# Performance work log

Measured on AMD Instinct MI355X. Metric: run time of the kernel, lower is better.

## Reference

```python
import jax, jax.numpy as jnp
import numpy as np

EMBED = 768
NUM_HEADS = 12
HEAD_DIM = EMBED // NUM_HEADS
SCALE = HEAD_DIM ** -0.5


def setup_inputs() -> dict:
    key = jax.random.key(0)
    ks = jax.random.split(key, 12)
    B, H, W = 1, 48, 48
    L = 2 * H - 1
    s = EMBED ** -0.5
    return {
        "hidden_states": jax.random.normal(ks[0], (B, H, W, EMBED), jnp.float32),
        "wq": jax.random.normal(ks[1], (EMBED, EMBED), jnp.float32) * s,
        "bq": jax.random.normal(ks[2], (EMBED,), jnp.float32) * 0.02,
        "wk": jax.random.normal(ks[3], (EMBED, EMBED), jnp.float32) * s,
        "bk": jax.random.normal(ks[4], (EMBED,), jnp.float32) * 0.02,
        "wv": jax.random.normal(ks[5], (EMBED, EMBED), jnp.float32) * s,
        "bv": jax.random.normal(ks[6], (EMBED,), jnp.float32) * 0.02,
        "wproj": jax.random.normal(ks[7], (EMBED, EMBED), jnp.float32) * s,
        "bproj": jax.random.normal(ks[8], (EMBED,), jnp.float32) * 0.02,
        "rel_pos_h": jax.random.normal(ks[9], (L, HEAD_DIM), jnp.float32) * 0.02,
        "rel_pos_w": jax.random.normal(ks[10], (L, HEAD_DIM), jnp.float32) * 0.02,
    }


def _get_rel_pos(q_size, k_size, rel_pos):
    # q_size == k_size here; table already has 2*size-1 entries (no interp)
    q = jnp.arange(q_size)[:, None]
    k = jnp.arange(k_size)[None, :]
    idx = q - k + (k_size - 1)  # (q_size, k_size)
    return rel_pos[idx]  # (q_size, k_size, head_dim)


def reference(hidden_states, wq, bq, wk, bk, wv, bv, wproj, bproj, rel_pos_h, rel_pos_w):
    B, H, W, C = hidden_states.shape
    nH, hd = NUM_HEADS, HEAD_DIM
    HW = H * W

    def proj_heads(w, b):
        # 1x1 conv == linear: (B,H,W,C) -> (B*nH, HW, hd)
        y = jnp.einsum("bhwc,oc->bhwo", hidden_states, w) + b
        return y.reshape(B, HW, nH, hd).transpose(0, 2, 1, 3).reshape(B * nH, HW, hd)

    q = proj_heads(wq, bq)
    k = proj_heads(wk, bk)
    v = proj_heads(wv, bv)

    scores = jnp.einsum("bqd,bkd->bqk", q * SCALE, k)  # (B*nH, HW, HW)

    Rh = _get_rel_pos(H, H, rel_pos_h)  # (H,H,hd)
    Rw = _get_rel_pos(W, W, rel_pos_w)  # (W,W,hd)
    qr = q.reshape(B * nH, H, W, hd)
    rel_h = jnp.einsum("bhwc,hkc->bhwk", qr, Rh)  # (B*nH,H,W,H)
    rel_w = jnp.einsum("bhwc,wkc->bhwk", qr, Rw)  # (B*nH,H,W,W)
    bias = rel_h[:, :, :, :, None] + rel_w[:, :, :, None, :]
    scores = scores + bias.reshape(B * nH, HW, HW)

    attn = jax.nn.softmax(scores.astype(jnp.float32), axis=-1).astype(q.dtype)
    out = jnp.einsum("bqk,bkd->bqd", attn, v)  # (B*nH, HW, hd)
    out = out.reshape(B, nH, H, W, hd).transpose(0, 2, 3, 1, 4).reshape(B, H, W, C)
    out = jnp.einsum("bhwc,oc->bhwo", out, wproj) + bproj
    return out, attn
```

## Files before the change

### kernel.cpp

```cpp
#include <hip/hip_runtime.h>
#include <math.h>

#define EMBED 768
#define NH 12
#define HD 64
#define HWTOK 2304
#define SCALE 0.125f

typedef unsigned short ushort_t;
typedef __attribute__((ext_vector_type(8))) short short8v;
typedef __attribute__((ext_vector_type(4))) short short4v;
typedef __attribute__((ext_vector_type(4))) float f32x4;

__device__ __forceinline__ unsigned short f2bf(float f) {
  unsigned u = __float_as_uint(f);
  u += 0x7fffu + ((u >> 16) & 1u);
  return (unsigned short)(u >> 16);
}
__device__ __forceinline__ float bf2f(unsigned short h) {
  return __uint_as_float(((unsigned)h) << 16);
}

__device__ __forceinline__ void split2(float a, float b, unsigned& hi, unsigned& lo) {
  unsigned ua = __float_as_uint(a), ub = __float_as_uint(b);
  unsigned ra = ua + 0x7fffu + ((ua >> 16) & 1u);
  unsigned rb = ub + 0x7fffu + ((ub >> 16) & 1u);
  float ha = __uint_as_float(ra & 0xffff0000u);
  float hb = __uint_as_float(rb & 0xffff0000u);
  hi = (ra >> 16) | (rb & 0xffff0000u);
  unsigned la = __float_as_uint(a - ha);
  unsigned lb = __float_as_uint(b - hb);
  lo = (la >> 16) | (lb & 0xffff0000u);
}

__global__ __launch_bounds__(256)
void split_kernel(const float* __restrict__ src, ushort_t* __restrict__ dh,
                  ushort_t* __restrict__ dl, int n4) {
  int i = blockIdx.x * 256 + threadIdx.x;
  int stride = gridDim.x * 256;
  for (; i < n4; i += stride) {
    float4 v = ((const float4*)src)[i];
    unsigned h0, l0, h1, l1;
    split2(v.x, v.y, h0, l0);
    split2(v.z, v.w, h1, l1);
    *(uint2*)&dh[(size_t)i * 4] = make_uint2(h0, h1);
    *(uint2*)&dl[(size_t)i * 4] = make_uint2(l0, l1);
  }
}

__device__ __forceinline__ void stage16(const float* __restrict__ src, char* dh, char* dl,
                                        int b0, int rs) {
  const float4* s4 = (const float4*)src;
  float4 f0 = s4[0], f1 = s4[1], f2 = s4[2], f3 = s4[3];
  uint4 H0, L0, H1, L1;
  split2(f0.x, f0.y, H0.x, L0.x); split2(f0.z, f0.w, H0.y, L0.y);
  split2(f1.x, f1.y, H0.z, L0.z); split2(f1.z, f1.w, H0.w, L0.w);
  split2(f2.x, f2.y, H1.x, L1.x); split2(f2.z, f2.w, H1.y, L1.y);
  split2(f3.x, f3.y, H1.z, L1.z); split2(f3.z, f3.w, H1.w, L1.w);
  *(uint4*)(dh + (b0 ^ rs))        = H0;
  *(uint4*)(dh + ((b0 + 16) ^ rs)) = H1;
  *(uint4*)(dl + (b0 ^ rs))        = L0;
  *(uint4*)(dl + ((b0 + 16) ^ rs)) = L1;
}

template<int IN_F32, int OUT_MODE>
__global__ __launch_bounds__(256)
void gemm_bf3(const ushort_t* __restrict__ Ah, const ushort_t* __restrict__ Al,
              const float* __restrict__ Af, const float* __restrict__ W,
              const float* __restrict__ bias, float* __restrict__ Y,
              ushort_t* __restrict__ Yh, ushort_t* __restrict__ Yl,
              int M, int N, int K) {
  __shared__ __align__(16) char smem[32768];

  const int tid  = threadIdx.x;
  const int w    = tid >> 6;
  const int lane = tid & 63;
  const int u    = lane >> 4;
  const int cc   = lane & 15;
  const int mw   = w >> 1, nw = w & 1;
  const int m0   = blockIdx.y * 64;
  const int n0   = blockIdx.x * 64;
  const int sr   = tid >> 2;
  const int sq   = tid & 3;
  const int srs  = (sr & 7) << 4;

  char* sAh_w = smem;
  char* sAl_w = smem + 8192;
  char* sWh_w = smem + 16384;
  char* sWl_w = smem + 24576;
  const int swzc = (cc & 7) << 4;

  f32x4 acc[2][2];
#pragma unroll
  for (int i = 0; i < 2; ++i)
#pragma unroll
    for (int j = 0; j < 2; ++j) acc[i][j] = (f32x4){0.f, 0.f, 0.f, 0.f};

  for (int k0 = 0; k0 < K; k0 += 64) {
    __syncthreads();
    if (IN_F32) {
      stage16(&Af[(size_t)(m0 + sr) * K + k0 + sq * 16],
              sAh_w + sr * 128, sAl_w + sr * 128, sq * 32, srs);
    } else {
      const ushort_t* ap = &Ah[(size_t)(m0 + sr) * K + k0 + sq * 16];
      const ushort_t* lp = &Al[(size_t)(m0 + sr) * K + k0 + sq * 16];
      uint4 h0 = *(const uint4*)ap;
      uint4 h1 = *(const uint4*)(ap + 8);
      uint4 l0 = *(const uint4*)lp;
      uint4 l1 = *(const uint4*)(lp + 8);
      *(uint4*)(sAh_w + sr * 128 + ((sq * 32) ^ srs))      = h0;
      *(uint4*)(sAh_w + sr * 128 + ((sq * 32 + 16) ^ srs)) = h1;
      *(uint4*)(sAl_w + sr * 128 + ((sq * 32) ^ srs))      = l0;
      *(uint4*)(sAl_w + sr * 128 + ((sq * 32 + 16) ^ srs)) = l1;
    }
    stage16(&W[(size_t)(n0 + sr) * K + k0 + sq * 16],
            sWh_w + sr * 128, sWl_w + sr * 128, sq * 32, srs);
    __syncthreads();

#pragma unroll
    for (int k2 = 0; k2 < 2; ++k2) {
      const int ko = k2 * 64;
      short8v a_h[2], a_l[2], b_h[2], b_l[2];
#pragma unroll
      for (int i = 0; i < 2; ++i) {
        int off = (32 * mw + 16 * i + cc) * 128 + ((u * 16 + ko) ^ swzc);
        a_h[i] = *(const short8v*)(sAh_w + off);
        a_l[i] = *(const short8v*)(sAl_w + off);
      }
#pragma unroll
      for (int j = 0; j < 2; ++j) {
        int off = (32 * nw + 16 * j + cc) * 128 + ((u * 16 + ko) ^ swzc);
        b_h[j] = *(const short8v*)(sWh_w + off);
        b_l[j] = *(const short8v*)(sWl_w + off);
      }
#pragma unroll
      for (int i = 0; i < 2; ++i)
#pragma unroll
        for (int j = 0; j < 2; ++j) {
          acc[i][j] = __builtin_amdgcn_mfma_f32_16x16x32_bf16(a_h[i], b_h[j], acc[i][j], 0, 0, 0);
          acc[i][j] = __builtin_amdgcn_mfma_f32_16x16x32_bf16(a_h[i], b_l[j], acc[i][j], 0, 0, 0);
          acc[i][j] = __builtin_amdgcn_mfma_f32_16x16x32_bf16(a_l[i], b_h[j], acc[i][j], 0, 0, 0);
        }
    }
  }

  __syncthreads();
  float* Cs = (float*)smem;
#pragma unroll
  for (int i = 0; i < 2; ++i)
#pragma unroll
    for (int j = 0; j < 2; ++j)
#pragma unroll
      for (int r = 0; r < 4; ++r)
        Cs[(32 * mw + 16 * i + 4 * u + r) * 68 + 32 * nw + 16 * j + cc] = acc[i][j][r];
  __syncthreads();

  {
    int rr = tid >> 2, cg = (tid & 3) * 16;
    float v[16];
#pragma unroll
    for (int e = 0; e < 4; ++e) {
      float4 cv = *(const float4*)&Cs[rr * 68 + cg + 4 * e];
      float4 bv = *(const float4*)&bias[n0 + cg + 4 * e];
      v[4 * e + 0] = cv.x + bv.x; v[4 * e + 1] = cv.y + bv.y;
      v[4 * e + 2] = cv.z + bv.z; v[4 * e + 3] = cv.w + bv.w;
    }
    if (OUT_MODE == 0) {
#pragma unroll
      for (int e = 0; e < 4; ++e)
        *(float4*)&Y[(size_t)(m0 + rr) * N + n0 + cg + 4 * e] =
            make_float4(v[4 * e], v[4 * e + 1], v[4 * e + 2], v[4 * e + 3]);
    } else {
      unsigned short hh[16], ll[16];
#pragma unroll
      for (int e = 0; e < 16; ++e) {
        hh[e] = f2bf(v[e]);
        ll[e] = f2bf(v[e] - bf2f(hh[e]));
      }
      size_t base = ((size_t)(n0 >> 6) * M + (m0 + rr)) * HD + cg;
      *(short8v*)&Yh[base]     = (short8v){(short)hh[0],(short)hh[1],(short)hh[2],(short)hh[3],
                                           (short)hh[4],(short)hh[5],(short)hh[6],(short)hh[7]};
      *(short8v*)&Yh[base + 8] = (short8v){(short)hh[8],(short)hh[9],(short)hh[10],(short)hh[11],
                                           (short)hh[12],(short)hh[13],(short)hh[14],(short)hh[15]};
      *(short8v*)&Yl[base]     = (short8v){(short)ll[0],(short)ll[1],(short)ll[2],(short)ll[3],
                                           (short)ll[4],(short)ll[5],(short)ll[6],(short)ll[7]};
      *(short8v*)&Yl[base + 8] = (short8v){(short)ll[8],(short)ll[9],(short)ll[10],(short)ll[11],
                                           (short)ll[12],(short)ll[13],(short)ll[14],(short)ll[15]};
    }
  }
}

__global__ __launch_bounds__(256, 2)
void attn_kernel(const ushort_t* __restrict__ Qh, const ushort_t* __restrict__ Ql,
                 const ushort_t* __restrict__ Kh, const ushort_t* __restrict__ Kl,
                 const ushort_t* __restrict__ Vh, const ushort_t* __restrict__ Vl,
                 const float* __restrict__ RPH, const float* __restrict__ RPW,
                 float* __restrict__ attn, float* __restrict__ headout) {
  const int f   = blockIdx.y * gridDim.x + blockIdx.x;
  const int lgl = (f & 7) * 54 + (f >> 3);
  const int h   = lgl / 36;
  const int q0  = (lgl - h * 36) * 64;
  const int tid = threadIdx.x;
  const int w = tid >> 6, lane = tid & 63, u = lane >> 4, c = lane & 15;

  __shared__ __align__(16) char smem[73728];
  ushort_t* Ksh = (ushort_t*)(smem);
  ushort_t* Ksl = (ushort_t*)(smem + 8192);
  ushort_t* Vsh = (ushort_t*)(smem + 16384);
  ushort_t* Vsl = (ushort_t*)(smem + 24576);
  float*   relhT = (float*)(smem + 32768);
  float*   relwT = (float*)(smem + 45056);
  char*    PsB   = smem + 57344;
  float*   Qstage= (float*)(smem + 57344);

  const size_t hb = (size_t)h * HWTOK * HD;

  {
    int r = tid >> 2, dg = (tid & 3) * 16;
    size_t gi = hb + (size_t)(q0 + r) * HD + dg;
    short8v a0 = *(const short8v*)&Qh[gi];
    short8v a1 = *(const short8v*)&Qh[gi + 8];
    short8v b0 = *(const short8v*)&Ql[gi];
    short8v b1 = *(const short8v*)&Ql[gi + 8];
    float* dst = &Qstage[r * 64 + dg];
#pragma unroll
    for (int m = 0; m < 8; ++m) {
      dst[m]     = bf2f((unsigned short)a0[m]) + bf2f((unsigned short)b0[m]);
      dst[m + 8] = bf2f((unsigned short)a1[m]) + bf2f((unsigned short)b1[m]);
    }
  }
  __syncthreads();

  for (int idx = tid; idx < 64 * 48; idx += 256) {
    int r  = idx / 48;
    int kk = idx - r * 48;
    int t  = q0 + r;
    int y  = t / 48;
    int x  = t - y * 48;
    const float4* qp = (const float4*)&Qstage[r * 64];
    const float4* rp = (const float4*)&RPH[(size_t)(y - kk + 47) * HD];
    const float4* wp = (const float4*)&RPW[(size_t)(x - kk + 47) * HD];
    float sh = 0.f, sw = 0.f;
#pragma unroll
    for (int dd = 0; dd < 16; ++dd) {
      float4 a = qp[dd], b = rp[dd], cc2 = wp[dd];
      sh += a.x*b.x + a.y*b.y + a.z*b.z + a.w*b.w;
      sw += a.x*cc2.x + a.y*cc2.y + a.z*cc2.z + a.w*cc2.w;
    }
    relhT[kk * 64 + r] = sh;
    relwT[kk * 64 + r] = sw;
  }
  __syncthreads();

  short8v qf[2][2];
  {
    int qrow = q0 + 16 * w + c;
    size_t base = hb + (size_t)qrow * HD + u * 8;
    qf[0][0] = *(const short8v*)&Qh[base];
    qf[1][0] = *(const short8v*)&Qh[base + 32];
    qf[0][1] = *(const short8v*)&Ql[base];
    qf[1][1] = *(const short8v*)&Ql[base + 32];
  }

  f32x4 acc_o[4];
#pragma unroll
  for (int i = 0; i < 4; ++i) acc_o[i] = (f32x4){0.f, 0.f, 0.f, 0.f};
  float rsum = 0.f;

  const int qlocal = 16 * w + c;
  float* attn_row = &attn[((size_t)h * HWTOK + q0 + qlocal) * HWTOK];
  const int swz = (c & 7) << 4;

  for (int kt0 = 0; kt0 < HWTOK; kt0 += 64) {
    __syncthreads();
    {
      int r = tid >> 2, dg = (tid & 3) * 16;
      size_t gi = hb + (size_t)(kt0 + r) * HD + dg;
      short8v k0 = *(const short8v*)&Kh[gi];
      short8v k1 = *(const short8v*)&Kh[gi + 8];
      short8v k2 = *(const short8v*)&Kl[gi];
      short8v k3 = *(const short8v*)&Kl[gi + 8];
      int rs = (r & 7) << 4;
      char* kr = (char*)Ksh + r * 128;
      *(short8v*)(kr + ((dg * 2) ^ rs))      = k0;
      *(short8v*)(kr + ((dg * 2 + 16) ^ rs)) = k1;
      kr = (char*)Ksl + r * 128;
      *(short8v*)(kr + ((dg * 2) ^ rs))      = k2;
      *(short8v*)(kr + ((dg * 2 + 16) ^ rs)) = k3;
    }
    {
      int t4 = ((tid >> 2) & 15) * 4;
      int d4 = ((tid & 3) + (tid >> 6) * 4) * 4;
      short4v rh[4], rl[4];
#pragma unroll
      for (int k2 = 0; k2 < 4; ++k2) {
        size_t gi = hb + (size_t)(kt0 + t4 + k2) * HD + d4;
        rh[k2] = *(const short4v*)&Vh[gi];
        rl[k2] = *(const short4v*)&Vl[gi];
      }
#pragma unroll
      for (int i2 = 0; i2 < 4; ++i2) {
        int d = d4 + i2;
        int off = (t4 * 2) ^ ((d & 7) << 4);
        *(short4v*)((char*)Vsh + d * 128 + off) =
            (short4v){rh[0][i2], rh[1][i2], rh[2][i2], rh[3][i2]};
        *(short4v*)((char*)Vsl + d * 128 + off) =
            (short4v){rl[0][i2], rl[1][i2], rl[2][i2], rl[3][i2]};
      }
    }
    __syncthreads();

#pragma unroll
    for (int s = 0; s < 4; ++s) {
      const char* krh = (const char*)Ksh + (16 * s + c) * 128;
      const char* krl = (const char*)Ksl + (16 * s + c) * 128;
      short8v ah0 = *(const short8v*)(krh + ((u * 16) ^ swz));
      short8v ah1 = *(const short8v*)(krh + ((64 + u * 16) ^ swz));
      short8v al0 = *(const short8v*)(krl + ((u * 16) ^ swz));
      short8v al1 = *(const short8v*)(krl + ((64 + u * 16) ^ swz));
      f32x4 acc = (f32x4){0.f, 0.f, 0.f, 0.f};
      acc = __builtin_amdgcn_mfma_f32_16x16x32_bf16(ah0, qf[0][0], acc, 0, 0, 0);
      acc = __builtin_amdgcn_mfma_f32_16x16x32_bf16(ah1, qf[1][0], acc, 0, 0, 0);
      acc = __builtin_amdgcn_mfma_f32_16x16x32_bf16(ah0, qf[0][1], acc, 0, 0, 0);
      acc = __builtin_amdgcn_mfma_f32_16x16x32_bf16(ah1, qf[1][1], acc, 0, 0, 0);
      acc = __builtin_amdgcn_mfma_f32_16x16x32_bf16(al0, qf[0][0], acc, 0, 0, 0);
      acc = __builtin_amdgcn_mfma_f32_16x16x32_bf16(al1, qf[1][0], acc, 0, 0, 0);

      int tb = kt0 + 16 * s + 4 * u;
      unsigned short hi4[4], lo4[4];
#pragma unroll
      for (int r2 = 0; r2 < 4; ++r2) {
        int t  = tb + r2;
        int ky = t / 48;
        int kx = t - ky * 48;
        float sv = acc[r2] * SCALE + relhT[ky * 64 + qlocal] + relwT[kx * 64 + qlocal];
        float e = __expf(sv);
        rsum += e;
        hi4[r2] = f2bf(e);
        lo4[r2] = f2bf(e - bf2f(hi4[r2]));
      }
      char* pb = PsB + w * 4096 + c * 128;
      int off = (32 * s + 8 * u) ^ swz;
      *(short4v*)(pb + off) =
          (short4v){(short)hi4[0], (short)hi4[1], (short)hi4[2], (short)hi4[3]};
      *(short4v*)(pb + 2048 + off) =
          (short4v){(short)lo4[0], (short)lo4[1], (short)lo4[2], (short)lo4[3]};
    }

    short8v pf00, pf01, pf10, pf11;
    {
      char* pb = PsB + w * 4096 + c * 128;
      pf00 = *(const short8v*)(pb + ((u * 16) ^ swz));
      pf10 = *(const short8v*)(pb + ((64 + u * 16) ^ swz));
      pf01 = *(const short8v*)(pb + 2048 + ((u * 16) ^ swz));
      pf11 = *(const short8v*)(pb + 2048 + ((64 + u * 16) ^ swz));
    }
#pragma unroll
    for (int sd = 0; sd < 4; ++sd) {
      const char* vrh = (const char*)Vsh + (16 * sd + c) * 128;
      const char* vrl = (const char*)Vsl + (16 * sd + c) * 128;
      short8v vh0 = *(const short8v*)(vrh + ((u * 16) ^ swz));
      short8v vh1 = *(const short8v*)(vrh + ((64 + u * 16) ^ swz));
      short8v vl0 = *(const short8v*)(vrl + ((u * 16) ^ swz));
      short8v vl1 = *(const short8v*)(vrl + ((64 + u * 16) ^ swz));
      f32x4 ao = acc_o[sd];
      ao = __builtin_amdgcn_mfma_f32_16x16x32_bf16(vh0, pf00, ao, 0, 0, 0);
      ao = __builtin_amdgcn_mfma_f32_16x16x32_bf16(vh1, pf10, ao, 0, 0, 0);
      ao = __builtin_amdgcn_mfma_f32_16x16x32_bf16(vh0, pf01, ao, 0, 0, 0);
      ao = __builtin_amdgcn_mfma_f32_16x16x32_bf16(vh1, pf11, ao, 0, 0, 0);
      ao = __builtin_amdgcn_mfma_f32_16x16x32_bf16(vl0, pf00, ao, 0, 0, 0);
      ao = __builtin_amdgcn_mfma_f32_16x16x32_bf16(vl1, pf10, ao, 0, 0, 0);
      acc_o[sd] = ao;
    }
  }

  float tot = rsum;
  tot += __shfl_xor(tot, 16, 64);
  tot += __shfl_xor(tot, 32, 64);
  const float inv = 1.f / tot;

  {
    int qrow = q0 + qlocal;
#pragma unroll
    for (int sd = 0; sd < 4; ++sd) {
      float4 o = make_float4(acc_o[sd][0] * inv, acc_o[sd][1] * inv,
                             acc_o[sd][2] * inv, acc_o[sd][3] * inv);
      *(float4*)&headout[(size_t)qrow * EMBED + h * HD + 16 * sd + 4 * u] = o;
    }
  }

  for (int kt0 = 0; kt0 < HWTOK; kt0 += 64) {
    __syncthreads();
    {
      int r = tid >> 2, dg = (tid & 3) * 16;
      size_t gi = hb + (size_t)(kt0 + r) * HD + dg;
      short8v k0 = *(const short8v*)&Kh[gi];
      short8v k1 = *(const short8v*)&Kh[gi + 8];
      short8v k2 = *(const short8v*)&Kl[gi];
      short8v k3 = *(const short8v*)&Kl[gi + 8];
      int rs = (r & 7) << 4;
      char* kr = (char*)Ksh + r * 128;
      *(short8v*)(kr + ((dg * 2) ^ rs))      = k0;
      *(short8v*)(kr + ((dg * 2 + 16) ^ rs)) = k1;
      kr = (char*)Ksl + r * 128;
      *(short8v*)(kr + ((dg * 2) ^ rs))      = k2;
      *(short8v*)(kr + ((dg * 2 + 16) ^ rs)) = k3;
    }
    __syncthreads();

#pragma unroll
    for (int s = 0; s < 4; ++s) {
      const char* krh = (const char*)Ksh + (16 * s + c) * 128;
      const char* krl = (const char*)Ksl + (16 * s + c) * 128;
      short8v ah0 = *(const short8v*)(krh + ((u * 16) ^ swz));
      short8v ah1 = *(const short8v*)(krh + ((64 + u * 16) ^ swz));
      short8v al0 = *(const short8v*)(krl + ((u * 16) ^ swz));
      short8v al1 = *(const short8v*)(krl + ((64 + u * 16) ^ swz));
      f32x4 acc = (f32x4){0.f, 0.f, 0.f, 0.f};
      acc = __builtin_amdgcn_mfma_f32_16x16x32_bf16(ah0, qf[0][0], acc, 0, 0, 0);
      acc = __builtin_amdgcn_mfma_f32_16x16x32_bf16(ah1, qf[1][0], acc, 0, 0, 0);
      acc = __builtin_amdgcn_mfma_f32_16x16x32_bf16(ah0, qf[0][1], acc, 0, 0, 0);
      acc = __builtin_amdgcn_mfma_f32_16x16x32_bf16(ah1, qf[1][1], acc, 0, 0, 0);
      acc = __builtin_amdgcn_mfma_f32_16x16x32_bf16(al0, qf[0][0], acc, 0, 0, 0);
      acc = __builtin_amdgcn_mfma_f32_16x16x32_bf16(al1, qf[1][0], acc, 0, 0, 0);

      int tb = kt0 + 16 * s + 4 * u;
      float pr[4];
#pragma unroll
      for (int r2 = 0; r2 < 4; ++r2) {
        int t  = tb + r2;
        int ky = t / 48;
        int kx = t - ky * 48;
        float sv = acc[r2] * SCALE + relhT[ky * 64 + qlocal] + relwT[kx * 64 + qlocal];
        pr[r2] = __expf(sv) * inv;
      }
      *(float4*)&attn_row[tb] = make_float4(pr[0], pr[1], pr[2], pr[3]);
    }
  }
}

extern "C" void kernel_launch(void* const* d_in, const int* in_sizes, int n_in,
                              void* d_out, int out_size, void* d_ws, size_t ws_size,
                              hipStream_t stream) {
  const float* hs    = (const float*)d_in[0];
  const float* wq    = (const float*)d_in[1];
  const float* bq    = (const float*)d_in[2];
  const float* wk    = (const float*)d_in[3];
  const float* bk    = (const float*)d_in[4];
  const float* wv    = (const float*)d_in[5];
  const float* bv    = (const float*)d_in[6];
  const float* wproj = (const float*)d_in[7];
  const float* bproj = (const float*)d_in[8];
  const float* rph   = (const float*)d_in[9];
  const float* rpw   = (const float*)d_in[10];

  float* out  = (float*)d_out;
  float* attn = out + (size_t)HWTOK * EMBED;

  const size_t QSZ = (size_t)NH * HWTOK * HD;

  char* wsb = (char*)d_ws;
  float*    hout = (float*)wsb;
  ushort_t* ah   = (ushort_t*)wsb;
  ushort_t* al   = ah + QSZ;
  ushort_t* qh   = (ushort_t*)(wsb + QSZ * 4);
  ushort_t* ql   = qh + QSZ;
  ushort_t* kh   = ql + QSZ;
  ushort_t* kl   = kh + QSZ;
  ushort_t* vh   = kl + QSZ;
  ushort_t* vl   = vh + QSZ;

  const int HS4 = (int)((size_t)HWTOK * EMBED / 4);

  split_kernel<<<1728, 256, 0, stream>>>(hs, ah, al, HS4);

  dim3 gg(EMBED / 64, HWTOK / 64);
  gemm_bf3<0, 1><<<gg, 256, 0, stream>>>(ah, al, nullptr, wq, bq, nullptr, qh, ql,
                                         HWTOK, EMBED, EMBED);
  gemm_bf3<0, 1><<<gg, 256, 0, stream>>>(ah, al, nullptr, wk, bk, nullptr, kh, kl,
                                         HWTOK, EMBED, EMBED);
  gemm_bf3<0, 1><<<gg, 256, 0, stream>>>(ah, al, nullptr, wv, bv, nullptr, vh, vl,
                                         HWTOK, EMBED, EMBED);

  attn_kernel<<<dim3(HWTOK / 64, NH), 256, 0, stream>>>(qh, ql, kh, kl, vh, vl,
                                                        rph, rpw, attn, hout);

  gemm_bf3<1, 0><<<gg, 256, 0, stream>>>(nullptr, nullptr, hout, wproj, bproj, out,
                                         nullptr, nullptr, HWTOK, EMBED, EMBED);
}
```

Before: 565.3 us.

## Fuse QKV GEMMs into one launch and register-prefetch tiles in GEMM and attention

Merges the three Q/K/V projection GEMMs into a single 1296-block launch, with an XCD-aware block remap that selects the weight and bias per block. Both the GEMM and the attention kernel now prefetch the next K/V or A/W tile into registers while the current tile is computed, overlapping global loads with MFMA work. The MFMA sequences are wrapped in s_setprio, and the GEMM gets launch_bounds occupancy 3. The cost is higher register pressure from the prefetch buffers, which could lower occupancy or cause spills.

Measured after the change: 522.0 us. -7.7%, faster.

```diff
diff --git a/kernel.cpp b/kernel.cpp
--- a/kernel.cpp
+++ b/kernel.cpp
@@ -48,74 +48,106 @@
   }
 }
 
-__device__ __forceinline__ void stage16(const float* __restrict__ src, char* dh, char* dl,
-                                        int b0, int rs) {
-  const float4* s4 = (const float4*)src;
-  float4 f0 = s4[0], f1 = s4[1], f2 = s4[2], f3 = s4[3];
-  uint4 H0, L0, H1, L1;
-  split2(f0.x, f0.y, H0.x, L0.x); split2(f0.z, f0.w, H0.y, L0.y);
-  split2(f1.x, f1.y, H0.z, L0.z); split2(f1.z, f1.w, H0.w, L0.w);
-  split2(f2.x, f2.y, H1.x, L1.x); split2(f2.z, f2.w, H1.y, L1.y);
-  split2(f3.x, f3.y, H1.z, L1.z); split2(f3.z, f3.w, H1.w, L1.w);
-  *(uint4*)(dh + (b0 ^ rs))        = H0;
-  *(uint4*)(dh + ((b0 + 16) ^ rs)) = H1;
-  *(uint4*)(dl + (b0 ^ rs))        = L0;
-  *(uint4*)(dl + ((b0 + 16) ^ rs)) = L1;
-}
-
-template<int IN_F32, int OUT_MODE>
-__global__ __launch_bounds__(256)
+template<int IN_F32, int OUT_MODE, int FUSED>
+__global__ __launch_bounds__(256, 3)
 void gemm_bf3(const ushort_t* __restrict__ Ah, const ushort_t* __restrict__ Al,
-              const float* __restrict__ Af, const float* __restrict__ W,
-              const float* __restrict__ bias, float* __restrict__ Y,
-              ushort_t* __restrict__ Yh, ushort_t* __restrict__ Yl,
+              const float* __restrict__ Af,
+              const float* __restrict__ W0, const float* __restrict__ W1,
+              const float* __restrict__ W2,
+              const float* __restrict__ b0, const float* __restrict__ b1,
+              const float* __restrict__ b2,
+              float* __restrict__ Y, ushort_t* __restrict__ Yh0,
               int M, int N, int K) {
   __shared__ __align__(16) char smem[32768];
 
   const int tid  = threadIdx.x;
+  const int g    = blockIdx.x;
+  int which, r;
+  if (FUSED) { int b = (g & 7) * 162 + (g >> 3); which = b / 432; r = b - which * 432; }
+  else       { int b = (g & 7) * 54  + (g >> 3); which = 0;       r = b; }
+  const float* W    = FUSED ? (which == 0 ? W0 : which == 1 ? W1 : W2) : W0;
+  const float* bias = FUSED ? (which == 0 ? b0 : which == 1 ? b1 : b2) : b0;
+  const int n0 = (r % 12) * 64;
+  const int m0 = (r / 12) * 64;
+
   const int w    = tid >> 6;
   const int lane = tid & 63;
   const int u    = lane >> 4;
   const int cc   = lane & 15;
   const int mw   = w >> 1, nw = w & 1;
-  const int m0   = blockIdx.y * 64;
-  const int n0   = blockIdx.x * 64;
   const int sr   = tid >> 2;
   const int sq   = tid & 3;
   const int srs  = (sr & 7) << 4;
 
-  char* sAh_w = smem;
-  char* sAl_w = smem + 8192;
-  char* sWh_w = smem + 16384;
-  char* sWl_w = smem + 24576;
+  char* sAh_ = smem;
+  char* sAl_ = smem + 8192;
+  char* sWh_ = smem + 16384;
+  char* sWl_ = smem + 24576;
   const int swzc = (cc & 7) << 4;
 
-  f32x4 acc[2][2];
-#pragma unroll
-  for (int i = 0; i < 2; ++i)
-#pragma unroll
-    for (int j = 0; j < 2; ++j) acc[i][j] = (f32x4){0.f, 0.f, 0.f, 0.f};
-
-  for (int k0 = 0; k0 < K; k0 += 64) {
-    __syncthreads();
+  uint4  pah0, pah1, pal0, pal1;
+  float4 paf0, paf1, paf2, paf3;
+  float4 pw0, pw1, pw2, pw3;
+
+  auto loadA = [&](int k0) {
     if (IN_F32) {
-      stage16(&Af[(size_t)(m0 + sr) * K + k0 + sq * 16],
-              sAh_w + sr * 128, sAl_w + sr * 128, sq * 32, srs);
+      const float4* s4 = (const float4*)&Af[(size_t)(m0 + sr) * K + k0 + sq * 16];
+      paf0 = s4[0]; paf1 = s4[1]; paf2 = s4[2]; paf3 = s4[3];
     } else {
       const ushort_t* ap = &Ah[(size_t)(m0 + sr) * K + k0 + sq * 16];
       const ushort_t* lp = &Al[(size_t)(m0 + sr) * K + k0 + sq * 16];
-      uint4 h0 = *(const uint4*)ap;
-      uint4 h1 = *(const uint4*)(ap + 8);
-      uint4 l0 = *(const uint4*)lp;
-      uint4 l1 = *(const uint4*)(lp + 8);
-      *(uint4*)(sAh_w + sr * 128 + ((sq * 32) ^ srs))      = h0;
-      *(uint4*)(sAh_w + sr * 128 + ((sq * 32 + 16) ^ srs)) = h1;
-      *(uint4*)(sAl_w + sr * 128 + ((sq * 32) ^ srs))      = l0;
-      *(uint4*)(sAl_w + sr * 128 + ((sq * 32 + 16) ^ srs)) = l1;
-    }
-    stage16(&W[(size_t)(n0 + sr) * K + k0 + sq * 16],
-            sWh_w + sr * 128, sWl_w + sr * 128, sq * 32, srs);
+      pah0 = *(const uint4*)ap; pah1 = *(const uint4*)(ap + 8);
+      pal0 = *(const uint4*)lp; pal1 = *(const uint4*)(lp + 8);
+    }
+  };
+  auto loadW = [&](int k0) {
+    const float4* s4 = (const float4*)&W[(size_t)(n0 + sr) * K + k0 + sq * 16];
+    pw0 = s4[0]; pw1 = s4[1]; pw2 = s4[2]; pw3 = s4[3];
+  };
+  auto storeStage = [&]() {
+    char* ar = sAh_ + sr * 128;
+    char* lr = sAl_ + sr * 128;
+    if (IN_F32) {
+      uint4 H0, L0, H1, L1;
+      split2(paf0.x, paf0.y, H0.x, L0.x); split2(paf0.z, paf0.w, H0.y, L0.y);
+      split2(paf1.x, paf1.y, H0.z, L0.z); split2(paf1.z, paf1.w, H0.w, L0.w);
+      split2(paf2.x, paf2.y, H1.x, L1.x); split2(paf2.z, paf2.w, H1.y, L1.y);
+      split2(paf3.x, paf3.y, H1.z, L1.z); split2(paf3.z, paf3.w, H1.w, L1.w);
+      *(uint4*)(ar + ((sq * 32) ^ srs))      = H0;
+      *(uint4*)(ar + ((sq * 32 + 16) ^ srs)) = H1;
+      *(uint4*)(lr + ((sq * 32) ^ srs))      = L0;
+      *(uint4*)(lr + ((sq * 32 + 16) ^ srs)) = L1;
+    } else {
+      *(uint4*)(ar + ((sq * 32) ^ srs))      = pah0;
+      *(uint4*)(ar + ((sq * 32 + 16) ^ srs)) = pah1;
+      *(uint4*)(lr + ((sq * 32) ^ srs))      = pal0;
+      *(uint4*)(lr + ((sq * 32 + 16) ^ srs)) = pal1;
+    }
+    uint4 H0, L0, H1, L1;
+    split2(pw0.x, pw0.y, H0.x, L0.x); split2(pw0.z, pw0.w, H0.y, L0.y);
+    split2(pw1.x, pw1.y, H0.z, L0.z); split2(pw1.z, pw1.w, H0.w, L0.w);
+    split2(pw2.x, pw2.y, H1.x, L1.x); split2(pw2.z, pw2.w, H1.y, L1.y);
+    split2(pw3.x, pw3.y, H1.z, L1.z); split2(pw3.z, pw3.w, H1.w, L1.w);
+    char* wr = sWh_ + sr * 128;
+    *(uint4*)(wr + ((sq * 32) ^ srs))      = H0;
+    *(uint4*)(wr + ((sq * 32 + 16) ^ srs)) = H1;
+    wr = sWl_ + sr * 128;
+    *(uint4*)(wr + ((sq * 32) ^ srs))      = L0;
+    *(uint4*)(wr + ((sq * 32 + 16) ^ srs)) = L1;
+  };
+
+  f32x4 acc[2][2];
+#pragma unroll
+  for (int i = 0; i < 2; ++i)
+#pragma unroll
+    for (int j = 0; j < 2; ++j) acc[i][j] = (f32x4){0.f, 0.f, 0.f, 0.f};
+
+  loadA(0); loadW(0);
+  for (int k0 = 0; k0 < K; k0 += 64) {
     __syncthreads();
+    storeStage();
+    __syncthreads();
+    if (k0 + 64 < K) { loadA(k0 + 64); loadW(k0 + 64); }
 
 #pragma unroll
     for (int k2 = 0; k2 < 2; ++k2) {
@@ -124,14 +156,14 @@
 #pragma unroll
       for (int i = 0; i < 2; ++i) {
         int off = (32 * mw + 16 * i + cc) * 128 + ((u * 16 + ko) ^ swzc);
-        a_h[i] = *(const short8v*)(sAh_w + off);
-        a_l[i] = *(const short8v*)(sAl_w + off);
+        a_h[i] = *(const short8v*)(sAh_ + off);
+        a_l[i] = *(const short8v*)(sAl_ + off);
       }
 #pragma unroll
       for (int j = 0; j < 2; ++j) {
         int off = (32 * nw + 16 * j + cc) * 128 + ((u * 16 + ko) ^ swzc);
-        b_h[j] = *(const short8v*)(sWh_w + off);
-        b_l[j] = *(const short8v*)(sWl_w + off);
+        b_h[j] = *(const short8v*)(sWh_ + off);
+        b_l[j] = *(const short8v*)(sWl_ + off);
       }
 #pragma unroll
       for (int i = 0; i < 2; ++i)
@@ -151,8 +183,8 @@
 #pragma unroll
     for (int j = 0; j < 2; ++j)
 #pragma unroll
-      for (int r = 0; r < 4; ++r)
-        Cs[(32 * mw + 16 * i + 4 * u + r) * 68 + 32 * nw + 16 * j + cc] = acc[i][j][r];
+      for (int rr2 = 0; rr2 < 4; ++rr2)
+        Cs[(32 * mw + 16 * i + 4 * u + rr2) * 68 + 32 * nw + 16 * j + cc] = acc[i][j][rr2];
   __syncthreads();
 
   {
@@ -171,6 +203,9 @@
         *(float4*)&Y[(size_t)(m0 + rr) * N + n0 + cg + 4 * e] =
             make_float4(v[4 * e], v[4 * e + 1], v[4 * e + 2], v[4 * e + 3]);
     } else {
+      const size_t MN = (size_t)M * N;
+      ushort_t* Yh = Yh0 + (size_t)which * 2 * MN;
+      ushort_t* Yl = Yh + MN;
       unsigned short hh[16], ll[16];
 #pragma unroll
       for (int e = 0; e < 16; ++e) {
@@ -215,6 +250,48 @@
 
   const size_t hb = (size_t)h * HWTOK * HD;
 
+  const int str = tid >> 2, sdg = (tid & 3) * 16;
+  const int vt4 = ((tid >> 2) & 15) * 4;
+  const int vd4 = ((tid & 3) + (tid >> 6) * 4) * 4;
+  short8v kA, kB, kC, kD;
+  short4v vrh[4], vrl[4];
+
+  auto loadK = [&](int kt0) {
+    size_t gi = hb + (size_t)(kt0 + str) * HD + sdg;
+    kA = *(const short8v*)&Kh[gi];
+    kB = *(const short8v*)&Kh[gi + 8];
+    kC = *(const short8v*)&Kl[gi];
+    kD = *(const short8v*)&Kl[gi + 8];
+  };
+  auto loadV = [&](int kt0) {
+#pragma unroll
+    for (int k2 = 0; k2 < 4; ++k2) {
+      size_t gi = hb + (size_t)(kt0 + vt4 + k2) * HD + vd4;
+      vrh[k2] = *(const short4v*)&Vh[gi];
+      vrl[k2] = *(const short4v*)&Vl[gi];
+    }
+  };
+  auto writeK = [&]() {
+    int rs = (str & 7) << 4;
+    char* kr = (char*)Ksh + str * 128;
+    *(short8v*)(kr + ((sdg * 2) ^ rs))      = kA;
+    *(short8v*)(kr + ((sdg * 2 + 16) ^ rs)) = kB;
+    kr = (char*)Ksl + str * 128;
+    *(short8v*)(kr + ((sdg * 2) ^ rs))      = kC;
+    *(short8v*)(kr + ((sdg * 2 + 16) ^ rs)) = kD;
+  };
+  auto writeV = [&]() {
+#pragma unroll
+    for (int i2 = 0; i2 < 4; ++i2) {
+      int d = vd4 + i2;
+      int off = (vt4 * 2) ^ ((d & 7) << 4);
+      *(short4v*)((char*)Vsh + d * 128 + off) =
+          (short4v){vrh[0][i2], vrh[1][i2], vrh[2][i2], vrh[3][i2]};
+      *(short4v*)((char*)Vsl + d * 128 + off) =
+          (short4v){vrl[0][i2], vrl[1][i2], vrl[2][i2], vrl[3][i2]};
+    }
+  };
+
   {
     int r = tid >> 2, dg = (tid & 3) * 16;
     size_t gi = hb + (size_t)(q0 + r) * HD + dg;
@@ -229,6 +306,7 @@
       dst[m + 8] = bf2f((unsigned short)a1[m]) + bf2f((unsigned short)b1[m]);
     }
   }
+  loadK(0); loadV(0);
   __syncthreads();
 
   for (int idx = tid; idx < 64 * 48; idx += 256) {
@@ -273,42 +351,9 @@
 
   for (int kt0 = 0; kt0 < HWTOK; kt0 += 64) {
     __syncthreads();
-    {
-      int r = tid >> 2, dg = (tid & 3) * 16;
-      size_t gi = hb + (size_t)(kt0 + r) * HD + dg;
-      short8v k0 = *(const short8v*)&Kh[gi];
-      short8v k1 = *(const short8v*)&Kh[gi + 8];
-      short8v k2 = *(const short8v*)&Kl[gi];
-      short8v k3 = *(const short8v*)&Kl[gi + 8];
-      int rs = (r & 7) << 4;
-      char* kr = (char*)Ksh + r * 128;
-      *(short8v*)(kr + ((dg * 2) ^ rs))      = k0;
-      *(short8v*)(kr + ((dg * 2 + 16) ^ rs)) = k1;
-      kr = (char*)Ksl + r * 128;
-      *(short8v*)(kr + ((dg * 2) ^ rs))      = k2;
-      *(short8v*)(kr + ((dg * 2 + 16) ^ rs)) = k3;
-    }
-    {
-      int t4 = ((tid >> 2) & 15) * 4;
-      int d4 = ((tid & 3) + (tid >> 6) * 4) * 4;
-      short4v rh[4], rl[4];
-#pragma unroll
-      for (int k2 = 0; k2 < 4; ++k2) {
-        size_t gi = hb + (size_t)(kt0 + t4 + k2) * HD + d4;
-        rh[k2] = *(const short4v*)&Vh[gi];
-        rl[k2] = *(const short4v*)&Vl[gi];
-      }
-#pragma unroll
-      for (int i2 = 0; i2 < 4; ++i2) {
-        int d = d4 + i2;
-        int off = (t4 * 2) ^ ((d & 7) << 4);
-        *(short4v*)((char*)Vsh + d * 128 + off) =
-            (short4v){rh[0][i2], rh[1][i2], rh[2][i2], rh[3][i2]};
-        *(short4v*)((char*)Vsl + d * 128 + off) =
-            (short4v){rl[0][i2], rl[1][i2], rl[2][i2], rl[3][i2]};
-      }
-    }
+    writeK(); writeV();
     __syncthreads();
+    if (kt0 + 64 < HWTOK) { loadK(kt0 + 64); loadV(kt0 + 64); }
 
 #pragma unroll
     for (int s = 0; s < 4; ++s) {
@@ -319,12 +364,14 @@
       short8v al0 = *(const short8v*)(krl + ((u * 16) ^ swz));
       short8v al1 = *(const short8v*)(krl + ((64 + u * 16) ^ swz));
       f32x4 acc = (f32x4){0.f, 0.f, 0.f, 0.f};
+      __builtin_amdgcn_s_setprio(1);
       acc = __builtin_amdgcn_mfma_f32_16x16x32_bf16(ah0, qf[0][0], acc, 0, 0, 0);
       acc = __builtin_amdgcn_mfma_f32_16x16x32_bf16(ah1, qf[1][0], acc, 0, 0, 0);
       acc = __builtin_amdgcn_mfma_f32_16x16x32_bf16(ah0, qf[0][1], acc, 0, 0, 0);
       acc = __builtin_amdgcn_mfma_f32_16x16x32_bf16(ah1, qf[1][1], acc, 0, 0, 0);
       acc = __builtin_amdgcn_mfma_f32_16x16x32_bf16(al0, qf[0][0], acc, 0, 0, 0);
       acc = __builtin_amdgcn_mfma_f32_16x16x32_bf16(al1, qf[1][0], acc, 0, 0, 0);
+      __builtin_amdgcn_s_setprio(0);
 
       int tb = kt0 + 16 * s + 4 * u;
       unsigned short hi4[4], lo4[4];
@@ -357,19 +404,21 @@
     }
 #pragma unroll
     for (int sd = 0; sd < 4; ++sd) {
-      const char* vrh = (const char*)Vsh + (16 * sd + c) * 128;
-      const char* vrl = (const char*)Vsl + (16 * sd + c) * 128;
-      short8v vh0 = *(const short8v*)(vrh + ((u * 16) ^ swz));
-      short8v vh1 = *(const short8v*)(vrh + ((64 + u * 16) ^ swz));
-      short8v vl0 = *(const short8v*)(vrl + ((u * 16) ^ swz));
-      short8v vl1 = *(const short8v*)(vrl + ((64 + u * 16) ^ swz));
+      const char* vrh_ = (const char*)Vsh + (16 * sd + c) * 128;
+      const char* vrl_ = (const char*)Vsl + (16 * sd + c) * 128;
+      short8v vh0 = *(const short8v*)(vrh_ + ((u * 16) ^ swz));
+      short8v vh1 = *(const short8v*)(vrh_ + ((64 + u * 16) ^ swz));
+      short8v vl0 = *(const short8v*)(vrl_ + ((u * 16) ^ swz));
+      short8v vl1 = *(const short8v*)(vrl_ + ((64 + u * 16) ^ swz));
       f32x4 ao = acc_o[sd];
+      __builtin_amdgcn_s_setprio(1);
       ao = __builtin_amdgcn_mfma_f32_16x16x32_bf16(vh0, pf00, ao, 0, 0, 0);
       ao = __builtin_amdgcn_mfma_f32_16x16x32_bf16(vh1, pf10, ao, 0, 0, 0);
       ao = __builtin_amdgcn_mfma_f32_16x16x32_bf16(vh0, pf01, ao, 0, 0, 0);
       ao = __builtin_amdgcn_mfma_f32_16x16x32_bf16(vh1, pf11, ao, 0, 0, 0);
       ao = __builtin_amdgcn_mfma_f32_16x16x32_bf16(vl0, pf00, ao, 0, 0, 0);
       ao = __builtin_amdgcn_mfma_f32_16x16x32_bf16(vl1, pf10, ao, 0, 0, 0);
+      __builtin_amdgcn_s_setprio(0);
       acc_o[sd] = ao;
     }
   }
@@ -389,24 +438,12 @@
     }
   }
 
+  loadK(0);
   for (int kt0 = 0; kt0 < HWTOK; kt0 += 64) {
     __syncthreads();
-    {
-      int r = tid >> 2, dg = (tid & 3) * 16;
-      size_t gi = hb + (size_t)(kt0 + r) * HD + dg;
-      short8v k0 = *(const short8v*)&Kh[gi];
-      short8v k1 = *(const short8v*)&Kh[gi + 8];
-      short8v k2 = *(const short8v*)&Kl[gi];
-      short8v k3 = *(const short8v*)&Kl[gi + 8];
-      int rs = (r & 7) << 4;
-      char* kr = (char*)Ksh + r * 128;
-      *(short8v*)(kr + ((dg * 2) ^ rs))      = k0;
-      *(short8v*)(kr + ((dg * 2 + 16) ^ rs)) = k1;
-      kr = (char*)Ksl + r * 128;
-      *(short8v*)(kr + ((dg * 2) ^ rs))      = k2;
-      *(short8v*)(kr + ((dg * 2 + 16) ^ rs)) = k3;
-    }
+    writeK();
     __syncthreads();
+    if (kt0 + 64 < HWTOK) loadK(kt0 + 64);
 
 #pragma unroll
     for (int s = 0; s < 4; ++s) {
@@ -417,12 +454,14 @@
       short8v al0 = *(const short8v*)(krl + ((u * 16) ^ swz));
       short8v al1 = *(const short8v*)(krl + ((64 + u * 16) ^ swz));
       f32x4 acc = (f32x4){0.f, 0.f, 0.f, 0.f};
+      __builtin_amdgcn_s_setprio(1);
       acc = __builtin_amdgcn_mfma_f32_16x16x32_bf16(ah0, qf[0][0], acc, 0, 0, 0);
       acc = __builtin_amdgcn_mfma_f32_16x16x32_bf16(ah1, qf[1][0], acc, 0, 0, 0);
       acc = __builtin_amdgcn_mfma_f32_16x16x32_bf16(ah0, qf[0][1], acc, 0, 0, 0);
       acc = __builtin_amdgcn_mfma_f32_16x16x32_bf16(ah1, qf[1][1], acc, 0, 0, 0);
       acc = __builtin_amdgcn_mfma_f32_16x16x32_bf16(al0, qf[0][0], acc, 0, 0, 0);
       acc = __builtin_amdgcn_mfma_f32_16x16x32_bf16(al1, qf[1][0], acc, 0, 0, 0);
+      __builtin_amdgcn_s_setprio(0);
 
       int tb = kt0 + 16 * s + 4 * u;
       float pr[4];
@@ -464,27 +503,24 @@
   ushort_t* ah   = (ushort_t*)wsb;
   ushort_t* al   = ah + QSZ;
   ushort_t* qh   = (ushort_t*)(wsb + QSZ * 4);
-  ushort_t* ql   = qh + QSZ;
-  ushort_t* kh   = ql + QSZ;
-  ushort_t* kl   = kh + QSZ;
-  ushort_t* vh   = kl + QSZ;
-  ushort_t* vl   = vh + QSZ;
 
   const int HS4 = (int)((size_t)HWTOK * EMBED / 4);
 
   split_kernel<<<1728, 256, 0, stream>>>(hs, ah, al, HS4);
 
-  dim3 gg(EMBED / 64, HWTOK / 64);
-  gemm_bf3<0, 1><<<gg, 256, 0, stream>>>(ah, al, nullptr, wq, bq, nullptr, qh, ql,
-                                         HWTOK, EMBED, EMBED);
-  gemm_bf3<0, 1><<<gg, 256, 0, stream>>>(ah, al, nullptr, wk, bk, nullptr, kh, kl,
-                                         HWTOK, EMBED, EMBED);
-  gemm_bf3<0, 1><<<gg, 256, 0, stream>>>(ah, al, nullptr, wv, bv, nullptr, vh, vl,
-                                         HWTOK, EMBED, EMBED);
-
+  gemm_bf3<0, 1, 1><<<1296, 256, 0, stream>>>(ah, al, nullptr, wq, wk, wv,
+                                              bq, bk, bv, nullptr, qh,
+                                              HWTOK, EMBED, EMBED);
+
+  ushort_t* ql = qh + QSZ;
+  ushort_t* kh = ql + QSZ;
+  ushort_t* kl = kh + QSZ;
+  ushort_t* vh = kl + QSZ;
+  ushort_t* vl = vh + QSZ;
   attn_kernel<<<dim3(HWTOK / 64, NH), 256, 0, stream>>>(qh, ql, kh, kl, vh, vl,
                                                         rph, rpw, attn, hout);
 
-  gemm_bf3<1, 0><<<gg, 256, 0, stream>>>(nullptr, nullptr, hout, wproj, bproj, out,
-                                         nullptr, nullptr, HWTOK, EMBED, EMBED);
-}
+  gemm_bf3<1, 0, 0><<<432, 256, 0, stream>>>(nullptr, nullptr, hout, wproj, nullptr,
+                                             nullptr, bproj, nullptr, nullptr, out,
+                                             nullptr, HWTOK, EMBED, EMBED);
+}
```
